# Kernel tuning notes

Hardware: AMD Instinct MI355X
Metric: run time of the kernel (lower is better)

The kernel has to match this reference:

```python
import jax, jax.numpy as jnp
import numpy as np

DIM = 256
NUM_HEADS = 8
HEAD_DIM = DIM // NUM_HEADS
SCALE = HEAD_DIM ** (-0.5)


def setup_inputs() -> dict:
    key = jax.random.key(0)
    k1, k2, k3, k4 = jax.random.split(key, 4)
    x = jax.random.normal(k1, (4, 1, DIM, 12, 12, 12), dtype=jnp.float32)
    w_qkv = jax.random.normal(k2, (3 * DIM, DIM), dtype=jnp.float32) * 0.02
    w_proj = jax.random.normal(k3, (DIM, DIM), dtype=jnp.float32) * 0.02
    b_proj = jax.random.normal(k4, (DIM,), dtype=jnp.float32) * 0.02
    return {"x": x, "w_qkv": w_qkv, "w_proj": w_proj, "b_proj": b_proj}


def reference(x, w_qkv, w_proj, b_proj):
    # x: [P=4, B, C, H, W, D]; 1x1x1 Conv3d == channel matmul
    P, B, C, H, W, D = x.shape
    N = H * W * D
    xf = x.reshape(P, B, C, N)                       # [P,B,C,N]
    qkv = jnp.einsum('pbcn,oc->pbon', xf, w_qkv)     # [P,B,3C,N]
    q, k, v = jnp.split(qkv, 3, axis=2)              # each [P,B,C,N]
    # fold batch*heads
    def heads(t):
        return t.reshape(P, B * NUM_HEADS, HEAD_DIM, N)
    q, k, v = heads(q) * SCALE, heads(k), heads(v)
    attn = jnp.einsum('phcm,phcn->phmn', q, k)       # [P,BH,N,N]
    attn = jax.nn.softmax(attn, axis=-1)
    out = jnp.einsum('phmn,phcn->phcm', attn, v)     # [P,BH,hd,N]
    out = out.reshape(P, B, C, N)
    out = jnp.einsum('pbcn,oc->pbon', out, w_proj) + b_proj[None, None, :, None]
    return out.reshape(P, B, C, H, W, D)
```

## Files before the change

### kernel.cpp

```cpp
#include <hip/hip_runtime.h>

#define NP 4
#define NH 8
#define HD 32
#define CD 256
#define NN 1728
#define NT_TILES 27
#define TILE_E 2048
#define SCALE_Q2 (0.17677669529663687f * 1.4426950408889634f)

typedef __bf16 bf16x8 __attribute__((ext_vector_type(8)));
typedef __bf16 bf16x4_t __attribute__((ext_vector_type(4)));
typedef short short4_t __attribute__((ext_vector_type(4)));
typedef float f32x4 __attribute__((ext_vector_type(4)));
typedef unsigned short ushort4_t __attribute__((ext_vector_type(4)));
typedef unsigned short ushort8_t __attribute__((ext_vector_type(8)));

__device__ __forceinline__ float bf2f(unsigned short u) {
  unsigned int v = ((unsigned int)u) << 16;
  return __builtin_bit_cast(float, v);
}
__device__ __forceinline__ unsigned short f2bf(float f) {
  unsigned int v = __builtin_bit_cast(unsigned int, f);
  unsigned int r = (v + 0x7FFFu + ((v >> 16) & 1u)) >> 16;
  return (unsigned short)r;
}

__global__ void k_prep(const float* __restrict__ x, unsigned short* __restrict__ xt,
                       const float* __restrict__ wqkv, const float* __restrict__ wproj,
                       unsigned short* __restrict__ wq_b, unsigned short* __restrict__ wp_b) {
  __shared__ __attribute__((aligned(16))) unsigned short tile[64 * 40];
  int bid = blockIdx.x;
  int t = threadIdx.x;
  if (bid >= 864) {
    int idx = ((bid - 864) * 256 + t) * 4;
    const float* src;
    unsigned short* dst;
    if (idx < 196608) { src = wqkv + idx; dst = wq_b + idx; }
    else { src = wproj + (idx - 196608); dst = wp_b + (idx - 196608); }
    float4 v = *(const float4*)src;
    ushort4_t o;
    o[0] = f2bf(v.x); o[1] = f2bf(v.y); o[2] = f2bf(v.z); o[3] = f2bf(v.w);
    *(ushort4_t*)dst = o;
    return;
  }
  int nb = (bid % 27) * 64, cb = ((bid / 27) & 7) * 32, p = bid / 216;
  {
    int c = t >> 3, ch = t & 7;
    const float* src = x + ((size_t)p * CD + cb + c) * NN + nb + ch * 8;
    float4 v0 = *(const float4*)src;
    float4 v1 = *(const float4*)(src + 4);
    int base = ch * 8;
    tile[(base + 0) * 40 + c] = f2bf(v0.x);
    tile[(base + 1) * 40 + c] = f2bf(v0.y);
    tile[(base + 2) * 40 + c] = f2bf(v0.z);
    tile[(base + 3) * 40 + c] = f2bf(v0.w);
    tile[(base + 4) * 40 + c] = f2bf(v1.x);
    tile[(base + 5) * 40 + c] = f2bf(v1.y);
    tile[(base + 6) * 40 + c] = f2bf(v1.z);
    tile[(base + 7) * 40 + c] = f2bf(v1.w);
  }
  __syncthreads();
  {
    int n = t >> 2, ch = t & 3;
    *(ushort8_t*)(xt + ((size_t)p * NN + nb + n) * CD + cb + ch * 8) =
        *(const ushort8_t*)&tile[n * 40 + ch * 8];
  }
}

__global__ void k_qkv(const unsigned short* __restrict__ xt,
                      const unsigned short* __restrict__ wqkv,
                      unsigned short* __restrict__ Qt, unsigned short* __restrict__ Kt,
                      unsigned short* __restrict__ Vv) {
  int p = blockIdx.z, ot = blockIdx.y, nt = blockIdx.x;
  int tid = threadIdx.x, w = tid >> 6, lane = tid & 63, l15 = lane & 15, g = lane >> 4;
  int nbase = nt * 64 + w * 16;
  f32x4 acc[4] = {};
  const unsigned short* arow = xt + ((size_t)p * NN + nbase + l15) * CD + g * 8;
  const unsigned short* wrow = wqkv + ((size_t)(ot * 64 + l15)) * CD + g * 8;
  for (int ks = 0; ks < 8; ks++) {
    bf16x8 a = *(const bf16x8*)(arow + ks * 32);
#pragma unroll
    for (int ob = 0; ob < 4; ob++) {
      bf16x8 b = *(const bf16x8*)(wrow + ob * 16 * CD + ks * 32);
      acc[ob] = __builtin_amdgcn_mfma_f32_16x16x32_bf16(a, b, acc[ob], 0, 0, 0);
    }
  }
#pragma unroll
  for (int ob = 0; ob < 4; ob++) {
    int o = ot * 64 + ob * 16 + l15;
    int wq = o >> 8, rem = o & 255, h = rem >> 5, cc = rem & 31;
    int ph = p * NH + h;
    size_t tb = (size_t)ph * (NT_TILES * TILE_E) + nt * TILE_E;
    if (wq == 0) {
      int nrow = nbase + g * 4;
      for (int r = 0; r < 4; r++)
        Qt[((size_t)ph * NN + nrow + r) * HD + cc] = f2bf(acc[ob][r] * SCALE_Q2);
    } else if (wq == 1) {
      for (int r = 0; r < 4; r++)
        Kt[tb + w * 512 + ((cc >> 3) * 16 + g * 4 + r) * 8 + (cc & 7)] = f2bf(acc[ob][r]);
    } else {
      ushort4_t vs;
      for (int r = 0; r < 4; r++) vs[r] = f2bf(acc[ob][r]);
      *(ushort4_t*)(Vv + tb + (w * 2 + (cc >> 4)) * 256 + (g * 16 + (cc & 15)) * 4) = vs;
    }
  }
}

__global__ __launch_bounds__(256) void k_attn(const unsigned short* __restrict__ Qt,
                                              const unsigned short* __restrict__ Kt,
                                              const unsigned short* __restrict__ Vv,
                                              unsigned short* __restrict__ op0,
                                              unsigned short* __restrict__ op1,
                                              float* __restrict__ Lp) {
  __shared__ __attribute__((aligned(16))) unsigned char lds[2 * 8192];
  int tid = threadIdx.x, w = tid >> 6, lane = tid & 63, l15 = lane & 15, g = lane >> 4;
  int mt = blockIdx.x, ph = blockIdx.y, z = blockIdx.z;
  int t0 = z * 14, tEnd = z ? NT_TILES : 14;
  bf16x8 qfrag = *(const bf16x8*)(Qt + ((size_t)ph * NN + mt * 64 + w * 16 + l15) * HD + g * 8);
  const unsigned short* ktb = Kt + (size_t)ph * (NT_TILES * TILE_E);
  const unsigned short* vbg = Vv + (size_t)ph * (NT_TILES * TILE_E);
  f32x4 lsum = {0.f, 0.f, 0.f, 0.f};
  f32x4 oacc[2] = {};
  f32x4 zacc = {0.f, 0.f, 0.f, 0.f};
  *(ushort8_t*)(lds + tid * 16) = *(const ushort8_t*)(ktb + t0 * TILE_E + tid * 8);
  *(ushort8_t*)(lds + 4096 + tid * 16) = *(const ushort8_t*)(vbg + t0 * TILE_E + tid * 8);
  __syncthreads();
  for (int nt = t0; nt < tEnd; nt++) {
    unsigned char* kbuf = lds + ((nt - t0) & 1) * 8192;
    unsigned char* vbuf = kbuf + 4096;
    unsigned char* bufN = lds + ((nt - t0 + 1) & 1) * 8192;
    ushort8_t kr, vr;
    bool pre = (nt + 1 < tEnd);
    if (pre) {
      kr = *(const ushort8_t*)(ktb + (nt + 1) * TILE_E + tid * 8);
      vr = *(const ushort8_t*)(vbg + (nt + 1) * TILE_E + tid * 8);
    }
    f32x4 s[4];
#pragma unroll
    for (int nf = 0; nf < 4; nf++) {
      bf16x8 kb = *(const bf16x8*)(kbuf + nf * 1024 + lane * 16);
      s[nf] = __builtin_amdgcn_mfma_f32_16x16x32_bf16(kb, qfrag, zacc, 0, 0, 0);
    }
    short4_t pa[4];
#pragma unroll
    for (int nf = 0; nf < 4; nf++) {
      f32x4 e;
#pragma unroll
      for (int r = 0; r < 4; r++) e[r] = __builtin_amdgcn_exp2f(s[nf][r]);
      lsum += e;
      bf16x4_t t;
#pragma unroll
      for (int r = 0; r < 4; r++) t[r] = (__bf16)e[r];
      pa[nf] = __builtin_bit_cast(short4_t, t);
    }
#pragma unroll
    for (int nf = 0; nf < 4; nf++) {
#pragma unroll
      for (int cb = 0; cb < 2; cb++) {
        ushort4_t vq = *(const ushort4_t*)(vbuf + (nf * 2 + cb) * 512 + lane * 8);
        short4_t va = __builtin_bit_cast(short4_t, vq);
        oacc[cb] = __builtin_amdgcn_mfma_f32_16x16x16bf16_1k(va, pa[nf], oacc[cb], 0, 0, 0);
      }
    }
    if (pre) {
      *(ushort8_t*)(bufN + tid * 16) = kr;
      *(ushort8_t*)(bufN + 4096 + tid * 16) = vr;
    }
    __syncthreads();
  }
  float total = lsum[0] + lsum[1] + lsum[2] + lsum[3];
  total += __shfl_xor(total, 16);
  total += __shfl_xor(total, 32);
  int m = mt * 64 + w * 16 + l15;
  unsigned short* op = z ? op1 : op0;
  if (g == 0) Lp[(size_t)z * 32 * NN + (size_t)ph * NN + m] = total;
#pragma unroll
  for (int cb = 0; cb < 2; cb++) {
    ushort4_t vs;
#pragma unroll
    for (int rr = 0; rr < 4; rr++) vs[rr] = f2bf(oacc[cb][rr]);
    *(ushort4_t*)(op + ((size_t)ph * NN + m) * 32 + cb * 16 + g * 4) = vs;
  }
}

__global__ void k_proj(const unsigned short* __restrict__ op0,
                       const unsigned short* __restrict__ op1,
                       const float* __restrict__ Lp,
                       const unsigned short* __restrict__ wproj,
                       const float* __restrict__ bproj,
                       float* __restrict__ out) {
  int p = blockIdx.z, ot = blockIdx.y, nt = blockIdx.x;
  int tid = threadIdx.x, w = tid >> 6, lane = tid & 63, l15 = lane & 15, g = lane >> 4;
  int nbase = nt * 64 + w * 16;
  int n = nbase + l15;
  f32x4 acc[4] = {};
  const unsigned short* wrow = wproj + ((size_t)(ot * 64 + l15)) * CD + g * 8;
  for (int ks = 0; ks < 8; ks++) {
    size_t r = (size_t)(p * NH + ks) * NN + n;
    float inv = 1.0f / (Lp[r] + Lp[(size_t)32 * NN + r]);
    ushort8_t a0 = *(const ushort8_t*)(op0 + r * 32 + g * 8);
    ushort8_t a1 = *(const ushort8_t*)(op1 + r * 32 + g * 8);
    bf16x8 a;
#pragma unroll
    for (int j = 0; j < 8; j++) a[j] = (__bf16)((bf2f(a0[j]) + bf2f(a1[j])) * inv);
#pragma unroll
    for (int ob = 0; ob < 4; ob++) {
      bf16x8 b = *(const bf16x8*)(wrow + ob * 16 * CD + ks * 32);
      acc[ob] = __builtin_amdgcn_mfma_f32_16x16x32_bf16(a, b, acc[ob], 0, 0, 0);
    }
  }
#pragma unroll
  for (int ob = 0; ob < 4; ob++) {
    int o = ot * 64 + ob * 16 + l15;
    float bias = bproj[o];
    int nrow = nbase + g * 4;
    float4 vs;
    vs.x = acc[ob][0] + bias;
    vs.y = acc[ob][1] + bias;
    vs.z = acc[ob][2] + bias;
    vs.w = acc[ob][3] + bias;
    *(float4*)(out + (size_t)p * CD * NN + (size_t)o * NN + nrow) = vs;
  }
}

extern "C" void kernel_launch(void* const* d_in, const int* in_sizes, int n_in,
                              void* d_out, int out_size, void* d_ws, size_t ws_size,
                              hipStream_t stream) {
  const float* x = (const float*)d_in[0];
  const float* wqkv = (const float*)d_in[1];
  const float* wproj = (const float*)d_in[2];
  const float* bproj = (const float*)d_in[3];
  float* out = (float*)d_out;
  unsigned short* ws = (unsigned short*)d_ws;
  const size_t SZ = (size_t)NP * NN * CD;
  unsigned short* xt = ws;
  unsigned short* Qt = ws + SZ;
  unsigned short* Kt = ws + 2 * SZ;
  unsigned short* Vv = ws + 3 * SZ;
  unsigned short* op1 = ws + 4 * SZ;
  unsigned short* wq_b = ws + 5 * SZ;
  unsigned short* wp_b = ws + 5 * SZ + 196608;
  float* Lp = (float*)(ws + 5 * SZ + 262144);
  unsigned short* op0 = xt;
  hipLaunchKernelGGL(k_prep, dim3(1120), dim3(256), 0, stream, x, xt, wqkv, wproj, wq_b, wp_b);
  hipLaunchKernelGGL(k_qkv, dim3(27, 12, NP), dim3(256), 0, stream, xt, wq_b, Qt, Kt, Vv);
  hipLaunchKernelGGL(k_attn, dim3(27, 32, 2), dim3(256), 0, stream, Qt, Kt, Vv, op0, op1, Lp);
  hipLaunchKernelGGL(k_proj, dim3(27, 4, NP), dim3(256), 0, stream, op0, op1, Lp, wp_b, bproj, out);
}
```

Before: 78.68 us.

## Stage QKV stores through LDS and process two KV tiles per sync in attention

```diff
diff --git a/kernel.cpp b/kernel.cpp
--- a/kernel.cpp
+++ b/kernel.cpp
@@ -68,10 +68,12 @@
   }
 }
 
-__global__ void k_qkv(const unsigned short* __restrict__ xt,
-                      const unsigned short* __restrict__ wqkv,
-                      unsigned short* __restrict__ Qt, unsigned short* __restrict__ Kt,
-                      unsigned short* __restrict__ Vv) {
+__global__ __launch_bounds__(256) void k_qkv(const unsigned short* __restrict__ xt,
+                                             const unsigned short* __restrict__ wqkv,
+                                             unsigned short* __restrict__ Qt,
+                                             unsigned short* __restrict__ Kt,
+                                             unsigned short* __restrict__ Vv) {
+  __shared__ __attribute__((aligned(16))) unsigned short smem[64 * 72];
   int p = blockIdx.z, ot = blockIdx.y, nt = blockIdx.x;
   int tid = threadIdx.x, w = tid >> 6, lane = tid & 63, l15 = lane & 15, g = lane >> 4;
   int nbase = nt * 64 + w * 16;
@@ -86,23 +88,38 @@
       acc[ob] = __builtin_amdgcn_mfma_f32_16x16x32_bf16(a, b, acc[ob], 0, 0, 0);
     }
   }
-#pragma unroll
-  for (int ob = 0; ob < 4; ob++) {
-    int o = ot * 64 + ob * 16 + l15;
-    int wq = o >> 8, rem = o & 255, h = rem >> 5, cc = rem & 31;
-    int ph = p * NH + h;
-    size_t tb = (size_t)ph * (NT_TILES * TILE_E) + nt * TILE_E;
-    if (wq == 0) {
-      int nrow = nbase + g * 4;
-      for (int r = 0; r < 4; r++)
-        Qt[((size_t)ph * NN + nrow + r) * HD + cc] = f2bf(acc[ob][r] * SCALE_Q2);
-    } else if (wq == 1) {
-      for (int r = 0; r < 4; r++)
-        Kt[tb + w * 512 + ((cc >> 3) * 16 + g * 4 + r) * 8 + (cc & 7)] = f2bf(acc[ob][r]);
-    } else {
+  int wq = ot >> 2;
+  if (wq == 2) {
+#pragma unroll
+    for (int ob = 0; ob < 4; ob++) {
+      int o = ot * 64 + ob * 16 + l15;
+      int rem = o & 255, h = rem >> 5, cc = rem & 31;
+      size_t tb = (size_t)(p * NH + h) * (NT_TILES * TILE_E) + nt * TILE_E;
       ushort4_t vs;
       for (int r = 0; r < 4; r++) vs[r] = f2bf(acc[ob][r]);
       *(ushort4_t*)(Vv + tb + (w * 2 + (cc >> 4)) * 256 + (g * 16 + (cc & 15)) * 4) = vs;
+    }
+    return;
+  }
+  float sc = (wq == 0) ? SCALE_Q2 : 1.0f;
+#pragma unroll
+  for (int ob = 0; ob < 4; ob++)
+    for (int r = 0; r < 4; r++)
+      smem[(w * 16 + g * 4 + r) * 72 + ob * 16 + l15] = f2bf(acc[ob][r] * sc);
+  __syncthreads();
+#pragma unroll
+  for (int i = 0; i < 2; i++) {
+    int cid = i * 256 + tid;
+    int row = cid >> 3, oc8 = cid & 7;
+    ushort8_t vv = *(const ushort8_t*)&smem[row * 72 + oc8 * 8];
+    int n = nt * 64 + row;
+    if (wq == 0) {
+      int h = ot * 2 + (oc8 >> 2), cc8 = (oc8 & 3) * 8;
+      *(ushort8_t*)(Qt + ((size_t)(p * NH + h) * NN + n) * HD + cc8) = vv;
+    } else {
+      int h = (ot - 4) * 2 + (oc8 >> 2), cc8 = (oc8 & 3) * 8;
+      size_t tb = (size_t)(p * NH + h) * (NT_TILES * TILE_E) + nt * TILE_E;
+      *(ushort8_t*)(Kt + tb + (row >> 4) * 512 + ((cc8 >> 3) * 16 + (row & 15)) * 8) = vv;
     }
   }
 }
@@ -113,34 +130,30 @@
                                               unsigned short* __restrict__ op0,
                                               unsigned short* __restrict__ op1,
                                               float* __restrict__ Lp) {
-  __shared__ __attribute__((aligned(16))) unsigned char lds[2 * 8192];
+  __shared__ __attribute__((aligned(16))) unsigned char lds[2 * 16384];
   int tid = threadIdx.x, w = tid >> 6, lane = tid & 63, l15 = lane & 15, g = lane >> 4;
   int mt = blockIdx.x, ph = blockIdx.y, z = blockIdx.z;
-  int t0 = z * 14, tEnd = z ? NT_TILES : 14;
+  int tA = z * 14;
+  int nPair = z ? 6 : 7;
+  bool tail = (z == 1);
   bf16x8 qfrag = *(const bf16x8*)(Qt + ((size_t)ph * NN + mt * 64 + w * 16 + l15) * HD + g * 8);
   const unsigned short* ktb = Kt + (size_t)ph * (NT_TILES * TILE_E);
   const unsigned short* vbg = Vv + (size_t)ph * (NT_TILES * TILE_E);
   f32x4 lsum = {0.f, 0.f, 0.f, 0.f};
   f32x4 oacc[2] = {};
   f32x4 zacc = {0.f, 0.f, 0.f, 0.f};
-  *(ushort8_t*)(lds + tid * 16) = *(const ushort8_t*)(ktb + t0 * TILE_E + tid * 8);
-  *(ushort8_t*)(lds + 4096 + tid * 16) = *(const ushort8_t*)(vbg + t0 * TILE_E + tid * 8);
+  const int so = tid * 16;
+  *(ushort8_t*)(lds + so)         = *(const ushort8_t*)(ktb + tA * TILE_E + tid * 8);
+  *(ushort8_t*)(lds + 4096 + so)  = *(const ushort8_t*)(ktb + (tA + 1) * TILE_E + tid * 8);
+  *(ushort8_t*)(lds + 8192 + so)  = *(const ushort8_t*)(vbg + tA * TILE_E + tid * 8);
+  *(ushort8_t*)(lds + 12288 + so) = *(const ushort8_t*)(vbg + (tA + 1) * TILE_E + tid * 8);
   __syncthreads();
-  for (int nt = t0; nt < tEnd; nt++) {
-    unsigned char* kbuf = lds + ((nt - t0) & 1) * 8192;
-    unsigned char* vbuf = kbuf + 4096;
-    unsigned char* bufN = lds + ((nt - t0 + 1) & 1) * 8192;
-    ushort8_t kr, vr;
-    bool pre = (nt + 1 < tEnd);
-    if (pre) {
-      kr = *(const ushort8_t*)(ktb + (nt + 1) * TILE_E + tid * 8);
-      vr = *(const ushort8_t*)(vbg + (nt + 1) * TILE_E + tid * 8);
-    }
+  auto compute = [&](const unsigned char* kb, const unsigned char* vb) {
     f32x4 s[4];
 #pragma unroll
     for (int nf = 0; nf < 4; nf++) {
-      bf16x8 kb = *(const bf16x8*)(kbuf + nf * 1024 + lane * 16);
-      s[nf] = __builtin_amdgcn_mfma_f32_16x16x32_bf16(kb, qfrag, zacc, 0, 0, 0);
+      bf16x8 kbv = *(const bf16x8*)(kb + nf * 1024 + lane * 16);
+      s[nf] = __builtin_amdgcn_mfma_f32_16x16x32_bf16(kbv, qfrag, zacc, 0, 0, 0);
     }
     short4_t pa[4];
 #pragma unroll
@@ -158,16 +171,44 @@
     for (int nf = 0; nf < 4; nf++) {
 #pragma unroll
       for (int cb = 0; cb < 2; cb++) {
-        ushort4_t vq = *(const ushort4_t*)(vbuf + (nf * 2 + cb) * 512 + lane * 8);
+        ushort4_t vq = *(const ushort4_t*)(vb + (nf * 2 + cb) * 512 + lane * 8);
         short4_t va = __builtin_bit_cast(short4_t, vq);
         oacc[cb] = __builtin_amdgcn_mfma_f32_16x16x16bf16_1k(va, pa[nf], oacc[cb], 0, 0, 0);
       }
     }
+  };
+  for (int pr = 0; pr < nPair; pr++) {
+    unsigned char* buf = lds + (pr & 1) * 16384;
+    unsigned char* bufN = lds + ((pr + 1) & 1) * 16384;
+    ushort8_t kr0, kr1, vr0, vr1;
+    bool pre = (pr + 1 < nPair);
+    bool preT = tail && (pr + 1 == nPair);
     if (pre) {
-      *(ushort8_t*)(bufN + tid * 16) = kr;
-      *(ushort8_t*)(bufN + 4096 + tid * 16) = vr;
+      int d = tA + 2 * (pr + 1);
+      kr0 = *(const ushort8_t*)(ktb + d * TILE_E + tid * 8);
+      kr1 = *(const ushort8_t*)(ktb + (d + 1) * TILE_E + tid * 8);
+      vr0 = *(const ushort8_t*)(vbg + d * TILE_E + tid * 8);
+      vr1 = *(const ushort8_t*)(vbg + (d + 1) * TILE_E + tid * 8);
+    } else if (preT) {
+      kr0 = *(const ushort8_t*)(ktb + 26 * TILE_E + tid * 8);
+      vr0 = *(const ushort8_t*)(vbg + 26 * TILE_E + tid * 8);
+    }
+    compute(buf, buf + 8192);
+    compute(buf + 4096, buf + 12288);
+    if (pre) {
+      *(ushort8_t*)(bufN + so) = kr0;
+      *(ushort8_t*)(bufN + 4096 + so) = kr1;
+      *(ushort8_t*)(bufN + 8192 + so) = vr0;
+      *(ushort8_t*)(bufN + 12288 + so) = vr1;
+    } else if (preT) {
+      *(ushort8_t*)(bufN + so) = kr0;
+      *(ushort8_t*)(bufN + 8192 + so) = vr0;
     }
     __syncthreads();
+  }
+  if (tail) {
+    unsigned char* buf = lds + (nPair & 1) * 16384;
+    compute(buf, buf + 8192);
   }
   float total = lsum[0] + lsum[1] + lsum[2] + lsum[3];
   total += __shfl_xor(total, 16);
@@ -184,12 +225,12 @@
   }
 }
 
-__global__ void k_proj(const unsigned short* __restrict__ op0,
-                       const unsigned short* __restrict__ op1,
-                       const float* __restrict__ Lp,
-                       const unsigned short* __restrict__ wproj,
-                       const float* __restrict__ bproj,
-                       float* __restrict__ out) {
+__global__ __launch_bounds__(256) void k_proj(const unsigned short* __restrict__ op0,
+                                              const unsigned short* __restrict__ op1,
+                                              const float* __restrict__ Lp,
+                                              const unsigned short* __restrict__ wproj,
+                                              const float* __restrict__ bproj,
+                                              float* __restrict__ out) {
   int p = blockIdx.z, ot = blockIdx.y, nt = blockIdx.x;
   int tid = threadIdx.x, w = tid >> 6, lane = tid & 63, l15 = lane & 15, g = lane >> 4;
   int nbase = nt * 64 + w * 16;
```

Measured after the change: 78.11 us. About the same (-0.7%).
